# Kernel tuning notes

Measured on AMD Instinct MI355X. Metric: run time of the kernel, lower is better.

The kernel has to match this reference:

```python
import jax, jax.numpy as jnp
import numpy as np

BLOCK = 16  # NVFP4 block size (per-block FP8 scale over 16 FP4 values)
FP4_GRID = jnp.array([0.0, 0.5, 1.0, 1.5, 2.0, 3.0, 4.0, 6.0], dtype=jnp.float32)
FP4_MIDS = jnp.array([0.25, 0.75, 1.25, 1.75, 2.5, 3.5, 5.0], dtype=jnp.float32)


def _quantize_fp4(v):
    # round-to-nearest onto the signed E2M1 grid {0,.5,1,1.5,2,3,4,6}
    a = jnp.clip(jnp.abs(v), 0.0, 6.0)
    idx = jnp.searchsorted(FP4_MIDS, a)
    return jnp.sign(v) * FP4_GRID[idx]


def _block_quantize(x):
    # returns (fp4 values, per-16-block scales) such that x ~= q * scale_blocked
    M, K = x.shape
    B = K // BLOCK
    xb = x.reshape(M, B, BLOCK)
    s = jnp.max(jnp.abs(xb), axis=-1) / 6.0 + 1e-8  # [M, B]
    q = _quantize_fp4(xb / s[:, :, None]).reshape(M, K)
    return q, s


def setup_inputs() -> dict:
    key = jax.random.key(0)
    k1, k2, k3 = jax.random.split(key, 3)
    M, K, N = 8192, 4096, 4096
    bsz, q_len = 4, 2048

    x_raw = jax.random.normal(k1, (M, K), dtype=jnp.float32)
    w_raw = jax.random.normal(k2, (N, K), dtype=jnp.float32) * 0.02

    # global weight scale as in NVFP4_reorder_quantize_w: max(w)/(448*6)
    scale_w_global = jnp.max(w_raw) / (448.0 * 6.0)
    qw, scale_w = _block_quantize(w_raw / scale_w_global)

    # activation global scale (produced upstream by the activation quantizer)
    scale_x_global = jnp.max(x_raw) / (448.0 * 6.0)
    qx, scale_x = _block_quantize(x_raw / scale_x_global)

    bias = jax.random.normal(k3, (N,), dtype=jnp.float32) * 0.01

    return {
        "qx": qx,                      # [M, K] FP4-grid values
        "scale_x": scale_x,            # [M, K//16] block scales
        "scale": scale_x_global,       # scalar global activation scale
        "qw": qw,                      # [N, K] FP4-grid values
        "scale_w": scale_w,            # [N, K//16] block scales
        "scale_w_global": scale_w_global,
        "bias": bias,                  # [N]
        "bsz": bsz,
        "q_len": q_len,
    }


def reference(qx, scale_x, scale, qw, scale_w, scale_w_global, bias, bsz, q_len):
    # Dequant-scaled GEMM: y = (qx .* sx)(qw .* sw)^T * (scale * scale_w_global) + bias
    M, K = qx.shape
    N = qw.shape[0]
    B = K // BLOCK
    xd = (qx.reshape(M, B, BLOCK) * scale_x[:, :, None]).reshape(M, K)
    wd = (qw.reshape(N, B, BLOCK) * scale_w[:, :, None]).reshape(N, K)
    y = jnp.einsum("mk,nk->mn", xd, wd) * (scale * scale_w_global)
    y = y + bias
    return y.reshape(bsz, q_len, -1)
```

## Files before the change

kernel.cpp:

```cpp
#include <hip/hip_runtime.h>
#include <cstdint>

#define K_DIM 4096
#define ROWB 13
#define NU64 (K_DIM / 64)

typedef __bf16 bf16x8 __attribute__((ext_vector_type(8)));
typedef float f32x4 __attribute__((ext_vector_type(4)));

__device__ inline unsigned short f2bf(float f) {
    union { float f; unsigned int u; } v; v.f = f;
    unsigned int u = v.u;
    return (unsigned short)((u + 0x7FFFu + ((u >> 16) & 1u)) >> 16);
}

__device__ __forceinline__ void gload16(const void* g, void* l) {
    __builtin_amdgcn_global_load_lds(
        (const __attribute__((address_space(1))) unsigned int*)g,
        (__attribute__((address_space(3))) unsigned int*)l,
        16, 0, 0);
}

__global__ __launch_bounds__(256) void dequant2_kernel(
        const float* __restrict__ qx, const float* __restrict__ sx,
        unsigned short* __restrict__ xd, long t8x,
        const float* __restrict__ qw, const float* __restrict__ sw,
        unsigned short* __restrict__ wd, long t8w) {
    long i = (long)blockIdx.x * blockDim.x + threadIdx.x;
    if (i >= t8x + t8w) return;
    const float* q; const float* s; unsigned short* o;
    if (i < t8x) { q = qx; s = sx; o = xd; }
    else         { q = qw; s = sw; o = wd; i -= t8x; }
    long e = i * 8;
    float sc = s[e >> 4];
    float4 v0 = *(const float4*)(q + e);
    float4 v1 = *(const float4*)(q + e + 4);
    union { unsigned short h[8]; uint4 u; } ov;
    ov.h[0] = f2bf(v0.x * sc); ov.h[1] = f2bf(v0.y * sc);
    ov.h[2] = f2bf(v0.z * sc); ov.h[3] = f2bf(v0.w * sc);
    ov.h[4] = f2bf(v1.x * sc); ov.h[5] = f2bf(v1.y * sc);
    ov.h[6] = f2bf(v1.z * sc); ov.h[7] = f2bf(v1.w * sc);
    *(uint4*)(o + e) = ov.u;
}


__global__ __launch_bounds__(512, 2) void gemm256_kernel(
        const unsigned short* __restrict__ A,
        const unsigned short* __restrict__ B,
        const float* __restrict__ sg1, const float* __restrict__ sg2,
        const float* __restrict__ bias,
        float* __restrict__ out, int M, int N) {
    __shared__ __align__(16) char lds[131072];

    const int tid  = threadIdx.x;
    const int lane = tid & 63;
    const int wid  = tid >> 6;
    const int wm   = wid >> 2;
    const int wn   = wid & 3;
    const int l15  = lane & 15;
    const int cb4  = lane >> 4;
    const int ax   = l15 & 7;

    const int nbn = N >> 8;
    const int nwg = (M >> 8) * nbn;
    const int cpx = nwg >> 3;
    const int bid = blockIdx.x;
    const int swz = (bid & 7) * cpx + (bid >> 3);
    const int tile_m = (swz / nbn) << 8;
    const int tile_n = (swz % nbn) << 8;

    const int scb = ((lane & 7) ^ (lane >> 3)) << 4;
    const char* gA0 = (const char*)A +
        ((size_t)(tile_m + 8 * wid + (lane >> 3)) << ROWB) + scb;
    const char* gB0 = (const char*)B +
        ((size_t)(tile_n + 8 * wid + (lane >> 3)) << ROWB) + scb;
    const int dA = wid * 1024;

    const int arow = wm * 128 + l15;
    const int aK0 = arow * 128 + ((cb4 ^ ax) << 4);
    const int aK1 = arow * 128 + (((4 + cb4) ^ ax) << 4);
    const int brow = wn * 64 + l15;
    const int bK0 = 32768 + brow * 128 + ((cb4 ^ ax) << 4);
    const int bK1 = 32768 + brow * 128 + (((4 + cb4) ^ ax) << 4);

    f32x4 acc[8][4];
#pragma unroll
    for (int mb = 0; mb < 8; ++mb)
#pragma unroll
        for (int nb = 0; nb < 4; ++nb) acc[mb][nb] = (f32x4){0.f, 0.f, 0.f, 0.f};

#pragma unroll
    for (int p = 0; p < 4; ++p) {
        gload16(gA0 + ((size_t)(p * 64) << ROWB), lds + p * 8192 + dA);
        gload16(gB0 + ((size_t)(p * 64) << ROWB), lds + 32768 + p * 8192 + dA);
    }
    asm volatile("s_waitcnt vmcnt(0)" ::: "memory");
    __builtin_amdgcn_s_barrier();

#define UNIT_BODY(U, CUR, STG) do {                                          \
    const int su  = ((U) + 1 < NU64) ? (U) + 1 : (NU64 - 1);                 \
    const size_t sub = (size_t)su << 7;                                      \
    _Pragma("unroll")                                                        \
    for (int p = 0; p < 4; ++p) {                                            \
        gload16(gA0 + ((size_t)(p * 64) << ROWB) + sub,                      \
                lds + (STG) + p * 8192 + dA);                                \
        gload16(gB0 + ((size_t)(p * 64) << ROWB) + sub,                      \
                lds + (STG) + 32768 + p * 8192 + dA);                        \
    }                                                                        \
    {                                                                        \
        bf16x8 afr[8], bfr[4];                                               \
        _Pragma("unroll")                                                    \
        for (int nb = 0; nb < 4; ++nb)                                       \
            bfr[nb] = *(const bf16x8*)(lds + (CUR) + bK0 + nb * 2048);       \
        _Pragma("unroll")                                                    \
        for (int mb = 0; mb < 8; ++mb)                                       \
            afr[mb] = *(const bf16x8*)(lds + (CUR) + aK0 + mb * 2048);       \
        __builtin_amdgcn_s_barrier();                                        \
        __builtin_amdgcn_s_setprio(1);                                       \
        _Pragma("unroll")                                                    \
        for (int mb = 0; mb < 8; ++mb)                                       \
            _Pragma("unroll")                                                \
            for (int nb = 0; nb < 4; ++nb)                                   \
                acc[mb][nb] = __builtin_amdgcn_mfma_f32_16x16x32_bf16(       \
                    afr[mb], bfr[nb], acc[mb][nb], 0, 0, 0);                 \
        __builtin_amdgcn_s_setprio(0);                                       \
    }                                                                        \
    {                                                                        \
        bf16x8 afr[8], bfr[4];                                               \
        _Pragma("unroll")                                                    \
        for (int nb = 0; nb < 4; ++nb)                                       \
            bfr[nb] = *(const bf16x8*)(lds + (CUR) + bK1 + nb * 2048);       \
        _Pragma("unroll")                                                    \
        for (int mb = 0; mb < 8; ++mb)                                       \
            afr[mb] = *(const bf16x8*)(lds + (CUR) + aK1 + mb * 2048);       \
        __builtin_amdgcn_s_barrier();                                        \
        __builtin_amdgcn_s_setprio(1);                                       \
        _Pragma("unroll")                                                    \
        for (int mb = 0; mb < 8; ++mb)                                       \
            _Pragma("unroll")                                                \
            for (int nb = 0; nb < 4; ++nb)                                   \
                acc[mb][nb] = __builtin_amdgcn_mfma_f32_16x16x32_bf16(       \
                    afr[mb], bfr[nb], acc[mb][nb], 0, 0, 0);                 \
        __builtin_amdgcn_s_setprio(0);                                       \
    }                                                                        \
    asm volatile("s_waitcnt vmcnt(0)" ::: "memory");                         \
    __builtin_amdgcn_s_barrier();                                            \
} while (0)

    for (int up = 0; up < NU64; up += 2) {
        UNIT_BODY(up,     0,     65536);
        UNIT_BODY(up + 1, 65536, 0);
    }
#undef UNIT_BODY

    const float gs = sg1[0] * sg2[0];
    const int row0 = tile_m + wm * 128 + (cb4 << 2);
    const int col0 = tile_n + wn * 64 + l15;
    float bv[4];
#pragma unroll
    for (int nb = 0; nb < 4; ++nb) bv[nb] = bias[col0 + nb * 16];
#pragma unroll
    for (int mb = 0; mb < 8; ++mb)
#pragma unroll
        for (int nb = 0; nb < 4; ++nb) {
            const int col = col0 + nb * 16;
#pragma unroll
            for (int j = 0; j < 4; ++j)
                out[(size_t)(row0 + mb * 16 + j) * N + col] =
                    acc[mb][nb][j] * gs + bv[nb];
        }
}

__global__ __launch_bounds__(256) void gemm_fused_kernel(
        const float* __restrict__ qx, const float* __restrict__ sx,
        const float* __restrict__ qw, const float* __restrict__ sw,
        const float* __restrict__ sg1, const float* __restrict__ sg2,
        const float* __restrict__ bias,
        float* __restrict__ out, int M, int N) {
    __shared__ __align__(16) unsigned short As[128 * 32];
    __shared__ __align__(16) unsigned short Bs[128 * 32];
    const int tid  = threadIdx.x;
    const int lane = tid & 63;
    const int wid  = tid >> 6;
    const int tile_n = blockIdx.x * 128;
    const int tile_m = blockIdx.y * 128;
    const int wm = wid >> 1, wn = wid & 1;
    f32x4 acc[16];
#pragma unroll
    for (int i = 0; i < 16; ++i) acc[i] = (f32x4){0.f, 0.f, 0.f, 0.f};
    const int l15 = lane & 15;
    const int lk  = (lane >> 4) * 8;
    for (int kt = 0; kt < K_DIM / 32; ++kt) {
#pragma unroll
        for (int cc = 0; cc < 2; ++cc) {
            const int c   = tid + cc * 256;
            const int row = c >> 2;
            const int col = (c & 3) * 8;
            const int gk  = kt * 32 + col;
            {
                const float* qp = qx + (long)(tile_m + row) * K_DIM + gk;
                float s = sx[(long)(tile_m + row) * (K_DIM / 16) + (gk >> 4)];
                float4 a0 = *(const float4*)qp;
                float4 a1 = *(const float4*)(qp + 4);
                union { unsigned short h[8]; uint4 u; } o;
                o.h[0] = f2bf(a0.x * s); o.h[1] = f2bf(a0.y * s);
                o.h[2] = f2bf(a0.z * s); o.h[3] = f2bf(a0.w * s);
                o.h[4] = f2bf(a1.x * s); o.h[5] = f2bf(a1.y * s);
                o.h[6] = f2bf(a1.z * s); o.h[7] = f2bf(a1.w * s);
                *(uint4*)&As[row * 32 + col] = o.u;
            }
            {
                const float* qp = qw + (long)(tile_n + row) * K_DIM + gk;
                float s = sw[(long)(tile_n + row) * (K_DIM / 16) + (gk >> 4)];
                float4 a0 = *(const float4*)qp;
                float4 a1 = *(const float4*)(qp + 4);
                union { unsigned short h[8]; uint4 u; } o;
                o.h[0] = f2bf(a0.x * s); o.h[1] = f2bf(a0.y * s);
                o.h[2] = f2bf(a0.z * s); o.h[3] = f2bf(a0.w * s);
                o.h[4] = f2bf(a1.x * s); o.h[5] = f2bf(a1.y * s);
                o.h[6] = f2bf(a1.z * s); o.h[7] = f2bf(a1.w * s);
                *(uint4*)&Bs[row * 32 + col] = o.u;
            }
        }
        __syncthreads();
        const unsigned short* pa = As + (wm * 64 + l15) * 32 + lk;
        const unsigned short* pb = Bs + (wn * 64 + l15) * 32 + lk;
        bf16x8 a[4], b[4];
#pragma unroll
        for (int i = 0; i < 4; ++i) {
            a[i] = *(const bf16x8*)(pa + i * 16 * 32);
            b[i] = *(const bf16x8*)(pb + i * 16 * 32);
        }
#pragma unroll
        for (int mi = 0; mi < 4; ++mi)
#pragma unroll
            for (int ni = 0; ni < 4; ++ni)
                acc[mi * 4 + ni] = __builtin_amdgcn_mfma_f32_16x16x32_bf16(
                    a[mi], b[ni], acc[mi * 4 + ni], 0, 0, 0);
        __syncthreads();
    }
    const float gs = sg1[0] * sg2[0];
    const int row0 = tile_m + wm * 64 + (lane >> 4) * 4;
    const int col0 = tile_n + wn * 64 + l15;
#pragma unroll
    for (int mi = 0; mi < 4; ++mi)
#pragma unroll
        for (int ni = 0; ni < 4; ++ni) {
            const int col = col0 + ni * 16;
            const float bv = bias[col];
#pragma unroll
            for (int j = 0; j < 4; ++j)
                out[(long)(row0 + mi * 16 + j) * N + col] =
                    acc[mi * 4 + ni][j] * gs + bv;
        }
}

extern "C" void kernel_launch(void* const* d_in, const int* in_sizes, int n_in,
                              void* d_out, int out_size, void* d_ws, size_t ws_size,
                              hipStream_t stream) {
    const float* qx   = (const float*)d_in[0];
    const float* sx   = (const float*)d_in[1];
    const float* sc   = (const float*)d_in[2];
    const float* qw   = (const float*)d_in[3];
    const float* sw   = (const float*)d_in[4];
    const float* swg  = (const float*)d_in[5];
    const float* bias = (const float*)d_in[6];
    float* out = (float*)d_out;

    const int M = in_sizes[0] / K_DIM;
    const int N = in_sizes[3] / K_DIM;

    const size_t needA = (size_t)M * K_DIM * sizeof(unsigned short);
    const size_t needB = (size_t)N * K_DIM * sizeof(unsigned short);

    if (ws_size >= needA + needB) {
        unsigned short* xd = (unsigned short*)d_ws;
        unsigned short* wd = (unsigned short*)((char*)d_ws + needA);
        long t8x = (long)M * K_DIM / 8;
        long t8w = (long)N * K_DIM / 8;
        long tot = t8x + t8w;
        dequant2_kernel<<<(int)((tot + 255) / 256), 256, 0, stream>>>(
            qx, sx, xd, t8x, qw, sw, wd, t8w);
        const int nwg = (M / 256) * (N / 256);
        gemm256_kernel<<<nwg, 512, 0, stream>>>(xd, wd, sc, swg, bias, out, M, N);
    } else {
        dim3 grid(N / 128, M / 128);
        gemm_fused_kernel<<<grid, 256, 0, stream>>>(
            qx, sx, qw, sw, sc, swg, bias, out, M, N);
    }
}
```

Before: 302.7 us.

## Split GEMM K-tile into four quadrant phases with interleaved prefetch loads

```diff
diff --git a/kernel.cpp b/kernel.cpp
--- a/kernel.cpp
+++ b/kernel.cpp
@@ -3,7 +3,7 @@
 
 #define K_DIM 4096
 #define ROWB 13
-#define NU64 (K_DIM / 64)
+#define NT   (K_DIM / 64)
 
 typedef __bf16 bf16x8 __attribute__((ext_vector_type(8)));
 typedef float f32x4 __attribute__((ext_vector_type(4)));
@@ -59,7 +59,9 @@
     const int wn   = wid & 3;
     const int l15  = lane & 15;
     const int cb4  = lane >> 4;
-    const int ax   = l15 & 7;
+    const int rx   = l15 & 7;
+    const int xk0  = (cb4 ^ rx) << 4;
+    const int xk1  = ((4 + cb4) ^ rx) << 4;
 
     const int nbn = N >> 8;
     const int nwg = (M >> 8) * nbn;
@@ -69,19 +71,18 @@
     const int tile_m = (swz / nbn) << 8;
     const int tile_n = (swz % nbn) << 8;
 
-    const int scb = ((lane & 7) ^ (lane >> 3)) << 4;
-    const char* gA0 = (const char*)A +
-        ((size_t)(tile_m + 8 * wid + (lane >> 3)) << ROWB) + scb;
-    const char* gB0 = (const char*)B +
-        ((size_t)(tile_n + 8 * wid + (lane >> 3)) << ROWB) + scb;
-    const int dA = wid * 1024;
-
-    const int arow = wm * 128 + l15;
-    const int aK0 = arow * 128 + ((cb4 ^ ax) << 4);
-    const int aK1 = arow * 128 + (((4 + cb4) ^ ax) << 4);
-    const int brow = wn * 64 + l15;
-    const int bK0 = 32768 + brow * 128 + ((cb4 ^ ax) << 4);
-    const int bK1 = 32768 + brow * 128 + (((4 + cb4) ^ ax) << 4);
+    const int scb = ((lane & 7) ^ ((lane >> 3) & 7)) << 4;
+    const char* gA1 = (const char*)A +
+        ((size_t)(tile_m + wm * 128 + wn * 16 + (lane >> 3)) << ROWB) + scb;
+    const char* gA2 = gA1 + ((size_t)64 << ROWB);
+    const char* gBs = (const char*)B +
+        ((size_t)(tile_n + wn * 64 + wm * 32 + (lane >> 3)) << ROWB) + scb;
+    const int dA1 = (wm * 128 + wn * 16) * 128;
+    const int dA2 = dA1 + 8192;
+    const int dB  = 32768 + (wn * 64 + wm * 32) * 128;
+
+    const int aB = (wm * 128 + l15) * 128;
+    const int bB = 32768 + (wn * 64 + l15) * 128;
 
     f32x4 acc[8][4];
 #pragma unroll
@@ -89,69 +90,127 @@
 #pragma unroll
         for (int nb = 0; nb < 4; ++nb) acc[mb][nb] = (f32x4){0.f, 0.f, 0.f, 0.f};
 
-#pragma unroll
-    for (int p = 0; p < 4; ++p) {
-        gload16(gA0 + ((size_t)(p * 64) << ROWB), lds + p * 8192 + dA);
-        gload16(gB0 + ((size_t)(p * 64) << ROWB), lds + 32768 + p * 8192 + dA);
-    }
+    gload16(gA1, lds + dA1);
+    gload16(gA1 + ((size_t)8 << ROWB), lds + dA1 + 1024);
+    gload16(gBs, lds + dB);
+    gload16(gBs + ((size_t)8 << ROWB), lds + dB + 1024);
+    gload16(gBs + ((size_t)16 << ROWB), lds + dB + 2048);
+    gload16(gBs + ((size_t)24 << ROWB), lds + dB + 3072);
+    gload16(gA2, lds + dA2);
+    gload16(gA2 + ((size_t)8 << ROWB), lds + dA2 + 1024);
     asm volatile("s_waitcnt vmcnt(0)" ::: "memory");
     __builtin_amdgcn_s_barrier();
 
-#define UNIT_BODY(U, CUR, STG) do {                                          \
-    const int su  = ((U) + 1 < NU64) ? (U) + 1 : (NU64 - 1);                 \
-    const size_t sub = (size_t)su << 7;                                      \
-    _Pragma("unroll")                                                        \
-    for (int p = 0; p < 4; ++p) {                                            \
-        gload16(gA0 + ((size_t)(p * 64) << ROWB) + sub,                      \
-                lds + (STG) + p * 8192 + dA);                                \
-        gload16(gB0 + ((size_t)(p * 64) << ROWB) + sub,                      \
-                lds + (STG) + 32768 + p * 8192 + dA);                        \
-    }                                                                        \
-    {                                                                        \
-        bf16x8 afr[8], bfr[4];                                               \
+#define TILE_BODY(T, CB, SB) do {                                            \
+    const int ts_ = ((T) + 1 < NT) ? (T) + 1 : NT - 1;                       \
+    const size_t tso = (size_t)ts_ * 128;                                    \
+    bf16x8 af[8], af2[8], bf[4], bf2[4];                                     \
+           \
+    _Pragma("unroll")                                                        \
+    for (int mb = 0; mb < 4; ++mb) {                                         \
+        af[mb * 2 + 0] = *(const bf16x8*)(lds + (CB) + aB + mb * 2048 + xk0);\
+        af[mb * 2 + 1] = *(const bf16x8*)(lds + (CB) + aB + mb * 2048 + xk1);\
+    }                                                                        \
+    _Pragma("unroll")                                                        \
+    for (int nb = 0; nb < 2; ++nb) {                                         \
+        bf[nb * 2 + 0] = *(const bf16x8*)(lds + (CB) + bB + nb * 2048 + xk0);\
+        bf[nb * 2 + 1] = *(const bf16x8*)(lds + (CB) + bB + nb * 2048 + xk1);\
+    }                                                                        \
+    gload16(gA1 + tso, lds + (SB) + dA1);                                    \
+    gload16(gA1 + tso + ((size_t)8 << ROWB), lds + (SB) + dA1 + 1024);       \
+    asm volatile("s_waitcnt lgkmcnt(8)" ::: "memory");                       \
+    __builtin_amdgcn_s_barrier();                                            \
+    asm volatile("s_waitcnt lgkmcnt(0)" ::: "memory");                       \
+    __builtin_amdgcn_s_setprio(1);                                           \
+    _Pragma("unroll")                                                        \
+    for (int mb = 0; mb < 4; ++mb)                                           \
         _Pragma("unroll")                                                    \
-        for (int nb = 0; nb < 4; ++nb)                                       \
-            bfr[nb] = *(const bf16x8*)(lds + (CUR) + bK0 + nb * 2048);       \
+        for (int nb = 0; nb < 2; ++nb)                                       \
+            _Pragma("unroll")                                                \
+            for (int ks = 0; ks < 2; ++ks)                                   \
+                acc[mb][nb] = __builtin_amdgcn_mfma_f32_16x16x32_bf16(       \
+                    af[mb * 2 + ks], bf[nb * 2 + ks], acc[mb][nb], 0, 0, 0); \
+    __builtin_amdgcn_s_setprio(0);                                           \
+    __builtin_amdgcn_s_barrier();                                            \
+                   \
+    _Pragma("unroll")                                                        \
+    for (int nb = 0; nb < 2; ++nb) {                                         \
+        bf2[nb * 2 + 0] =                                                    \
+            *(const bf16x8*)(lds + (CB) + bB + 4096 + nb * 2048 + xk0);      \
+        bf2[nb * 2 + 1] =                                                    \
+            *(const bf16x8*)(lds + (CB) + bB + 4096 + nb * 2048 + xk1);      \
+    }                                                                        \
+    gload16(gBs + tso, lds + (SB) + dB);                                     \
+    gload16(gBs + tso + ((size_t)8 << ROWB), lds + (SB) + dB + 1024);        \
+    __builtin_amdgcn_s_barrier();                                            \
+    asm volatile("s_waitcnt lgkmcnt(0)" ::: "memory");                       \
+    __builtin_amdgcn_s_setprio(1);                                           \
+    _Pragma("unroll")                                                        \
+    for (int mb = 0; mb < 4; ++mb)                                           \
         _Pragma("unroll")                                                    \
-        for (int mb = 0; mb < 8; ++mb)                                       \
-            afr[mb] = *(const bf16x8*)(lds + (CUR) + aK0 + mb * 2048);       \
-        __builtin_amdgcn_s_barrier();                                        \
-        __builtin_amdgcn_s_setprio(1);                                       \
+        for (int nb = 0; nb < 2; ++nb)                                       \
+            _Pragma("unroll")                                                \
+            for (int ks = 0; ks < 2; ++ks)                                   \
+                acc[mb][2 + nb] = __builtin_amdgcn_mfma_f32_16x16x32_bf16(   \
+                    af[mb * 2 + ks], bf2[nb * 2 + ks], acc[mb][2 + nb],      \
+                    0, 0, 0);                                                \
+    __builtin_amdgcn_s_setprio(0);                                           \
+    asm volatile("s_waitcnt vmcnt(4)" ::: "memory");                         \
+    __builtin_amdgcn_s_barrier();                                            \
+                   \
+    _Pragma("unroll")                                                        \
+    for (int mb = 0; mb < 4; ++mb) {                                         \
+        af2[mb * 2 + 0] =                                                    \
+            *(const bf16x8*)(lds + (CB) + aB + 8192 + mb * 2048 + xk0);      \
+        af2[mb * 2 + 1] =                                                    \
+            *(const bf16x8*)(lds + (CB) + aB + 8192 + mb * 2048 + xk1);      \
+    }                                                                        \
+    gload16(gBs + tso + ((size_t)16 << ROWB), lds + (SB) + dB + 2048);       \
+    gload16(gBs + tso + ((size_t)24 << ROWB), lds + (SB) + dB + 3072);       \
+    __builtin_amdgcn_s_barrier();                                            \
+    asm volatile("s_waitcnt lgkmcnt(0)" ::: "memory");                       \
+    __builtin_amdgcn_s_setprio(1);                                           \
+    _Pragma("unroll")                                                        \
+    for (int mb = 0; mb < 4; ++mb)                                           \
         _Pragma("unroll")                                                    \
-        for (int mb = 0; mb < 8; ++mb)                                       \
+        for (int nb = 0; nb < 2; ++nb)                                       \
             _Pragma("unroll")                                                \
-            for (int nb = 0; nb < 4; ++nb)                                   \
-                acc[mb][nb] = __builtin_amdgcn_mfma_f32_16x16x32_bf16(       \
-                    afr[mb], bfr[nb], acc[mb][nb], 0, 0, 0);                 \
-        __builtin_amdgcn_s_setprio(0);                                       \
-    }                                                                        \
-    {                                                                        \
-        bf16x8 afr[8], bfr[4];                                               \
+            for (int ks = 0; ks < 2; ++ks)                                   \
+                acc[4 + mb][2 + nb] = __builtin_amdgcn_mfma_f32_16x16x32_bf16(\
+                    af2[mb * 2 + ks], bf2[nb * 2 + ks], acc[4 + mb][2 + nb], \
+                    0, 0, 0);                                                \
+    __builtin_amdgcn_s_setprio(0);                                           \
+    __builtin_amdgcn_s_barrier();                                            \
+                  \
+    _Pragma("unroll")                                                        \
+    for (int nb = 0; nb < 2; ++nb) {                                         \
+        bf[nb * 2 + 0] = *(const bf16x8*)(lds + (CB) + bB + nb * 2048 + xk0);\
+        bf[nb * 2 + 1] = *(const bf16x8*)(lds + (CB) + bB + nb * 2048 + xk1);\
+    }                                                                        \
+    gload16(gA2 + tso, lds + (SB) + dA2);                                    \
+    gload16(gA2 + tso + ((size_t)8 << ROWB), lds + (SB) + dA2 + 1024);       \
+    __builtin_amdgcn_s_barrier();                                            \
+    asm volatile("s_waitcnt lgkmcnt(0)" ::: "memory");                       \
+    __builtin_amdgcn_s_setprio(1);                                           \
+    _Pragma("unroll")                                                        \
+    for (int mb = 0; mb < 4; ++mb)                                           \
         _Pragma("unroll")                                                    \
-        for (int nb = 0; nb < 4; ++nb)                                       \
-            bfr[nb] = *(const bf16x8*)(lds + (CUR) + bK1 + nb * 2048);       \
-        _Pragma("unroll")                                                    \
-        for (int mb = 0; mb < 8; ++mb)                                       \
-            afr[mb] = *(const bf16x8*)(lds + (CUR) + aK1 + mb * 2048);       \
-        __builtin_amdgcn_s_barrier();                                        \
-        __builtin_amdgcn_s_setprio(1);                                       \
-        _Pragma("unroll")                                                    \
-        for (int mb = 0; mb < 8; ++mb)                                       \
+        for (int nb = 0; nb < 2; ++nb)                                       \
             _Pragma("unroll")                                                \
-            for (int nb = 0; nb < 4; ++nb)                                   \
-                acc[mb][nb] = __builtin_amdgcn_mfma_f32_16x16x32_bf16(       \
-                    afr[mb], bfr[nb], acc[mb][nb], 0, 0, 0);                 \
-        __builtin_amdgcn_s_setprio(0);                                       \
-    }                                                                        \
-    asm volatile("s_waitcnt vmcnt(0)" ::: "memory");                         \
+            for (int ks = 0; ks < 2; ++ks)                                   \
+                acc[4 + mb][nb] = __builtin_amdgcn_mfma_f32_16x16x32_bf16(   \
+                    af2[mb * 2 + ks], bf[nb * 2 + ks], acc[4 + mb][nb],      \
+                    0, 0, 0);                                                \
+    __builtin_amdgcn_s_setprio(0);                                           \
+    asm volatile("s_waitcnt vmcnt(2)" ::: "memory");                         \
     __builtin_amdgcn_s_barrier();                                            \
 } while (0)
 
-    for (int up = 0; up < NU64; up += 2) {
-        UNIT_BODY(up,     0,     65536);
-        UNIT_BODY(up + 1, 65536, 0);
+    for (int t = 0; t < NT; t += 2) {
+        TILE_BODY(t,     0,     65536);
+        TILE_BODY(t + 1, 65536, 0);
     }
-#undef UNIT_BODY
+#undef TILE_BODY
 
     const float gs = sg1[0] * sg2[0];
     const int row0 = tile_m + wm * 128 + (cb4 << 2);
```

Measured after the change: 279.3 us. 1.08x faster.
